# Optimization experiments

Hardware: AMD Instinct MI355X
Metric: run time of the kernel (lower is better)

## Reference

```python
import jax, jax.numpy as jnp
import numpy as np

IN_F, HID, OUT_F, N_HID = 3, 5, 1, 256
OMEGA0 = 30.0


def setup_inputs() -> dict:
    key = jax.random.key(0)
    ks = jax.random.split(key, 7)
    N = 524288
    coords = jax.random.uniform(ks[0], (N, IN_F), dtype=jnp.float32, minval=-1.0, maxval=1.0)
    # first layer init: U(-1/in, 1/in)
    W_first = jax.random.uniform(ks[1], (HID, IN_F), dtype=jnp.float32,
                                 minval=-1.0 / IN_F, maxval=1.0 / IN_F)
    b_first = jax.random.uniform(ks[2], (HID,), dtype=jnp.float32, minval=-1.0, maxval=1.0) / np.sqrt(IN_F)
    # hidden layers: U(-sqrt(6/in)/omega, sqrt(6/in)/omega)
    bnd = np.sqrt(6.0 / HID) / OMEGA0
    W_hidden = jax.random.uniform(ks[3], (N_HID, HID, HID), dtype=jnp.float32, minval=-bnd, maxval=bnd)
    b_hidden = jax.random.uniform(ks[4], (N_HID, HID), dtype=jnp.float32, minval=-1.0, maxval=1.0) / np.sqrt(HID)
    W_final = jax.random.uniform(ks[5], (OUT_F, HID), dtype=jnp.float32, minval=-bnd, maxval=bnd)
    b_final = jax.random.uniform(ks[6], (OUT_F,), dtype=jnp.float32, minval=-1.0, maxval=1.0) / np.sqrt(HID)
    return {"coords": coords, "W_first": W_first, "b_first": b_first,
            "W_hidden": W_hidden, "b_hidden": b_hidden,
            "W_final": W_final, "b_final": b_final}


def siren_forward(coords, W_first, b_first, W_hidden, b_hidden, W_final, b_final):
    # first SineLayer
    x = jnp.sin(OMEGA0 * (coords @ W_first.T + b_first))  # [N, HID]

    # 256 hidden SineLayers via scan over stacked weights
    def step(x, wb):
        w, b = wb  # w: [HID, HID], b: [HID]
        return jnp.sin(OMEGA0 * (x @ w.T + b)), None

    x, _ = jax.lax.scan(step, x, (W_hidden, b_hidden))
    # outermost linear (no sine)
    return x @ W_final.T + b_final  # [N, OUT_F]


def reference(coords, W_first, b_first, W_hidden, b_hidden, W_final, b_final):
    out = siren_forward(coords, W_first, b_first, W_hidden, b_hidden, W_final, b_final)
    # torch module returns (output, coords); coords is just the input passthrough
    return (out, coords)
```

## Files before the change

### kernel.cpp

```cpp
#include <hip/hip_runtime.h>
#include <math.h>


#define SIREN_HID 5
#define SIREN_NLAYERS 256

#define SIREN_REV 4.774648292756860f

__device__ __forceinline__ float siren_sin30(float z) {
    float t = z * SIREN_REV;
    return __builtin_amdgcn_sinf(__builtin_amdgcn_fractf(t));
}

__global__ __launch_bounds__(256)
void siren_fwd(const float* __restrict__ coords,
               const float* __restrict__ Wf,
               const float* __restrict__ bf,
               const float* __restrict__ Wh,
               const float* __restrict__ bh,
               const float* __restrict__ Wfin,
               const float* __restrict__ bfin,
               float* __restrict__ out, int N)
{
    int i = blockIdx.x * blockDim.x + threadIdx.x;
    if (i >= N) return;

    float c0 = coords[3 * i + 0];
    float c1 = coords[3 * i + 1];
    float c2 = coords[3 * i + 2];

    float h0, h1, h2, h3, h4;
    {
        float t0 = fmaf(c2, Wf[0 * 3 + 2], fmaf(c1, Wf[0 * 3 + 1], fmaf(c0, Wf[0 * 3 + 0], bf[0])));
        float t1 = fmaf(c2, Wf[1 * 3 + 2], fmaf(c1, Wf[1 * 3 + 1], fmaf(c0, Wf[1 * 3 + 0], bf[1])));
        float t2 = fmaf(c2, Wf[2 * 3 + 2], fmaf(c1, Wf[2 * 3 + 1], fmaf(c0, Wf[2 * 3 + 0], bf[2])));
        float t3 = fmaf(c2, Wf[3 * 3 + 2], fmaf(c1, Wf[3 * 3 + 1], fmaf(c0, Wf[3 * 3 + 0], bf[3])));
        float t4 = fmaf(c2, Wf[4 * 3 + 2], fmaf(c1, Wf[4 * 3 + 1], fmaf(c0, Wf[4 * 3 + 0], bf[4])));
        h0 = siren_sin30(t0);
        h1 = siren_sin30(t1);
        h2 = siren_sin30(t2);
        h3 = siren_sin30(t3);
        h4 = siren_sin30(t4);
    }

#pragma unroll 4
    for (int l = 0; l < SIREN_NLAYERS; ++l) {
        const float* w = Wh + l * (SIREN_HID * SIREN_HID);
        const float* b = bh + l * SIREN_HID;
        float t0 = fmaf(h4, w[ 4], fmaf(h3, w[ 3], fmaf(h2, w[ 2], fmaf(h1, w[ 1], fmaf(h0, w[ 0], b[0])))));
        float t1 = fmaf(h4, w[ 9], fmaf(h3, w[ 8], fmaf(h2, w[ 7], fmaf(h1, w[ 6], fmaf(h0, w[ 5], b[1])))));
        float t2 = fmaf(h4, w[14], fmaf(h3, w[13], fmaf(h2, w[12], fmaf(h1, w[11], fmaf(h0, w[10], b[2])))));
        float t3 = fmaf(h4, w[19], fmaf(h3, w[18], fmaf(h2, w[17], fmaf(h1, w[16], fmaf(h0, w[15], b[3])))));
        float t4 = fmaf(h4, w[24], fmaf(h3, w[23], fmaf(h2, w[22], fmaf(h1, w[21], fmaf(h0, w[20], b[4])))));
        h0 = siren_sin30(t0);
        h1 = siren_sin30(t1);
        h2 = siren_sin30(t2);
        h3 = siren_sin30(t3);
        h4 = siren_sin30(t4);
    }

    float o = fmaf(h4, Wfin[4], fmaf(h3, Wfin[3], fmaf(h2, Wfin[2], fmaf(h1, Wfin[1], fmaf(h0, Wfin[0], bfin[0])))));
    out[i] = o;

    float* oc = out + N;
    oc[3 * i + 0] = c0;
    oc[3 * i + 1] = c1;
    oc[3 * i + 2] = c2;
}

extern "C" void kernel_launch(void* const* d_in, const int* in_sizes, int n_in,
                              void* d_out, int out_size, void* d_ws, size_t ws_size,
                              hipStream_t stream) {
    const float* coords = (const float*)d_in[0];
    const float* Wf     = (const float*)d_in[1];
    const float* bf     = (const float*)d_in[2];
    const float* Wh     = (const float*)d_in[3];
    const float* bh     = (const float*)d_in[4];
    const float* Wfin   = (const float*)d_in[5];
    const float* bfin   = (const float*)d_in[6];

    int N = in_sizes[0] / 3;
    float* out = (float*)d_out;

    dim3 block(256);
    dim3 grid((N + 255) / 256);
    hipLaunchKernelGGL(siren_fwd, grid, block, 0, stream,
                       coords, Wf, bf, Wh, bh, Wfin, bfin, out, N);
}
```

Measured before the change: 170.8 us.

## Prescale weights by omega/2pi in a prep kernel and process two points per thread

A new prep kernel folds the omega0/(2π) factor into all first-layer and hidden weights and biases. It stores them in a workspace padded to 32 floats per layer. The main kernel then calls the hardware sin directly on the pre-activations, dropping the per-neuron multiply and fract. Each thread now evaluates two coordinates, which shares the weight loads and raises instruction-level parallelism, but it adds a second kernel launch and relies on v_sin handling unreduced arguments within its valid range.

```diff
diff --git a/kernel.cpp b/kernel.cpp
--- a/kernel.cpp
+++ b/kernel.cpp
@@ -4,68 +4,100 @@
 
 #define SIREN_HID 5
 #define SIREN_NLAYERS 256
-
 #define SIREN_REV 4.774648292756860f
 
-__device__ __forceinline__ float siren_sin30(float z) {
-    float t = z * SIREN_REV;
-    return __builtin_amdgcn_sinf(__builtin_amdgcn_fractf(t));
+__global__ __launch_bounds__(256)
+void siren_prep(const float* __restrict__ Wf, const float* __restrict__ bf,
+                const float* __restrict__ Wh, const float* __restrict__ bh,
+                float* __restrict__ ws)
+{
+    int t = blockIdx.x * blockDim.x + threadIdx.x;
+    const int total = SIREN_NLAYERS * 32;
+    for (int idx = t; idx < total; idx += gridDim.x * blockDim.x) {
+        int l = idx >> 5;
+        int k = idx & 31;
+        float v = 0.0f;
+        if (k < 25)      v = Wh[l * 25 + k] * SIREN_REV;
+        else if (k < 30) v = bh[l * 5 + (k - 25)] * SIREN_REV;
+        ws[idx] = v;
+    }
+    if (t < 15) ws[total + t]      = Wf[t] * SIREN_REV;
+    if (t < 5)  ws[total + 15 + t] = bf[t] * SIREN_REV;
 }
 
 __global__ __launch_bounds__(256)
-void siren_fwd(const float* __restrict__ coords,
-               const float* __restrict__ Wf,
-               const float* __restrict__ bf,
-               const float* __restrict__ Wh,
-               const float* __restrict__ bh,
-               const float* __restrict__ Wfin,
-               const float* __restrict__ bfin,
-               float* __restrict__ out, int N)
+void siren_fwd3(const float* __restrict__ coords,
+                const float* __restrict__ lw,
+                const float* __restrict__ fw,
+                const float* __restrict__ Wfin,
+                const float* __restrict__ bfin,
+                float* __restrict__ out, int N)
 {
     int i = blockIdx.x * blockDim.x + threadIdx.x;
-    if (i >= N) return;
+    const int M = N >> 1;
+    i = (i < M) ? i : (M - 1);
 
-    float c0 = coords[3 * i + 0];
-    float c1 = coords[3 * i + 1];
-    float c2 = coords[3 * i + 2];
+    const float* cp = coords + 6 * i;
+    float a0 = cp[0], a1 = cp[1], a2 = cp[2];
+    float b0 = cp[3], b1 = cp[4], b2 = cp[5];
 
-    float h0, h1, h2, h3, h4;
+    float ha0, ha1, ha2, ha3, ha4;
+    float hb0, hb1, hb2, hb3, hb4;
     {
-        float t0 = fmaf(c2, Wf[0 * 3 + 2], fmaf(c1, Wf[0 * 3 + 1], fmaf(c0, Wf[0 * 3 + 0], bf[0])));
-        float t1 = fmaf(c2, Wf[1 * 3 + 2], fmaf(c1, Wf[1 * 3 + 1], fmaf(c0, Wf[1 * 3 + 0], bf[1])));
-        float t2 = fmaf(c2, Wf[2 * 3 + 2], fmaf(c1, Wf[2 * 3 + 1], fmaf(c0, Wf[2 * 3 + 0], bf[2])));
-        float t3 = fmaf(c2, Wf[3 * 3 + 2], fmaf(c1, Wf[3 * 3 + 1], fmaf(c0, Wf[3 * 3 + 0], bf[3])));
-        float t4 = fmaf(c2, Wf[4 * 3 + 2], fmaf(c1, Wf[4 * 3 + 1], fmaf(c0, Wf[4 * 3 + 0], bf[4])));
-        h0 = siren_sin30(t0);
-        h1 = siren_sin30(t1);
-        h2 = siren_sin30(t2);
-        h3 = siren_sin30(t3);
-        h4 = siren_sin30(t4);
+        float s0 = fw[ 0], s1 = fw[ 1], s2 = fw[ 2], t0 = fw[15];
+        float s3 = fw[ 3], s4 = fw[ 4], s5 = fw[ 5], t1 = fw[16];
+        float s6 = fw[ 6], s7 = fw[ 7], s8 = fw[ 8], t2 = fw[17];
+        float s9 = fw[ 9], sA = fw[10], sB = fw[11], t3 = fw[18];
+        float sC = fw[12], sD = fw[13], sE = fw[14], t4 = fw[19];
+        float za0 = fmaf(a2, s2, fmaf(a1, s1, fmaf(a0, s0, t0)));
+        float za1 = fmaf(a2, s5, fmaf(a1, s4, fmaf(a0, s3, t1)));
+        float za2 = fmaf(a2, s8, fmaf(a1, s7, fmaf(a0, s6, t2)));
+        float za3 = fmaf(a2, sB, fmaf(a1, sA, fmaf(a0, s9, t3)));
+        float za4 = fmaf(a2, sE, fmaf(a1, sD, fmaf(a0, sC, t4)));
+        float zb0 = fmaf(b2, s2, fmaf(b1, s1, fmaf(b0, s0, t0)));
+        float zb1 = fmaf(b2, s5, fmaf(b1, s4, fmaf(b0, s3, t1)));
+        float zb2 = fmaf(b2, s8, fmaf(b1, s7, fmaf(b0, s6, t2)));
+        float zb3 = fmaf(b2, sB, fmaf(b1, sA, fmaf(b0, s9, t3)));
+        float zb4 = fmaf(b2, sE, fmaf(b1, sD, fmaf(b0, sC, t4)));
+        ha0 = __builtin_amdgcn_sinf(za0); hb0 = __builtin_amdgcn_sinf(zb0);
+        ha1 = __builtin_amdgcn_sinf(za1); hb1 = __builtin_amdgcn_sinf(zb1);
+        ha2 = __builtin_amdgcn_sinf(za2); hb2 = __builtin_amdgcn_sinf(zb2);
+        ha3 = __builtin_amdgcn_sinf(za3); hb3 = __builtin_amdgcn_sinf(zb3);
+        ha4 = __builtin_amdgcn_sinf(za4); hb4 = __builtin_amdgcn_sinf(zb4);
     }
 
-#pragma unroll 4
+#pragma unroll 2
     for (int l = 0; l < SIREN_NLAYERS; ++l) {
-        const float* w = Wh + l * (SIREN_HID * SIREN_HID);
-        const float* b = bh + l * SIREN_HID;
-        float t0 = fmaf(h4, w[ 4], fmaf(h3, w[ 3], fmaf(h2, w[ 2], fmaf(h1, w[ 1], fmaf(h0, w[ 0], b[0])))));
-        float t1 = fmaf(h4, w[ 9], fmaf(h3, w[ 8], fmaf(h2, w[ 7], fmaf(h1, w[ 6], fmaf(h0, w[ 5], b[1])))));
-        float t2 = fmaf(h4, w[14], fmaf(h3, w[13], fmaf(h2, w[12], fmaf(h1, w[11], fmaf(h0, w[10], b[2])))));
-        float t3 = fmaf(h4, w[19], fmaf(h3, w[18], fmaf(h2, w[17], fmaf(h1, w[16], fmaf(h0, w[15], b[3])))));
-        float t4 = fmaf(h4, w[24], fmaf(h3, w[23], fmaf(h2, w[22], fmaf(h1, w[21], fmaf(h0, w[20], b[4])))));
-        h0 = siren_sin30(t0);
-        h1 = siren_sin30(t1);
-        h2 = siren_sin30(t2);
-        h3 = siren_sin30(t3);
-        h4 = siren_sin30(t4);
+        const float* w = lw + l * 32;
+        float p0 = w[25], p1 = w[26], p2 = w[27], p3 = w[28], p4 = w[29];
+        float za0 = fmaf(ha4, w[ 4], fmaf(ha3, w[ 3], fmaf(ha2, w[ 2], fmaf(ha1, w[ 1], fmaf(ha0, w[ 0], p0)))));
+        float zb0 = fmaf(hb4, w[ 4], fmaf(hb3, w[ 3], fmaf(hb2, w[ 2], fmaf(hb1, w[ 1], fmaf(hb0, w[ 0], p0)))));
+        float za1 = fmaf(ha4, w[ 9], fmaf(ha3, w[ 8], fmaf(ha2, w[ 7], fmaf(ha1, w[ 6], fmaf(ha0, w[ 5], p1)))));
+        float zb1 = fmaf(hb4, w[ 9], fmaf(hb3, w[ 8], fmaf(hb2, w[ 7], fmaf(hb1, w[ 6], fmaf(hb0, w[ 5], p1)))));
+        float za2 = fmaf(ha4, w[14], fmaf(ha3, w[13], fmaf(ha2, w[12], fmaf(ha1, w[11], fmaf(ha0, w[10], p2)))));
+        float zb2 = fmaf(hb4, w[14], fmaf(hb3, w[13], fmaf(hb2, w[12], fmaf(hb1, w[11], fmaf(hb0, w[10], p2)))));
+        float za3 = fmaf(ha4, w[19], fmaf(ha3, w[18], fmaf(ha2, w[17], fmaf(ha1, w[16], fmaf(ha0, w[15], p3)))));
+        float zb3 = fmaf(hb4, w[19], fmaf(hb3, w[18], fmaf(hb2, w[17], fmaf(hb1, w[16], fmaf(hb0, w[15], p3)))));
+        float za4 = fmaf(ha4, w[24], fmaf(ha3, w[23], fmaf(ha2, w[22], fmaf(ha1, w[21], fmaf(ha0, w[20], p4)))));
+        float zb4 = fmaf(hb4, w[24], fmaf(hb3, w[23], fmaf(hb2, w[22], fmaf(hb1, w[21], fmaf(hb0, w[20], p4)))));
+        ha0 = __builtin_amdgcn_sinf(za0); hb0 = __builtin_amdgcn_sinf(zb0);
+        ha1 = __builtin_amdgcn_sinf(za1); hb1 = __builtin_amdgcn_sinf(zb1);
+        ha2 = __builtin_amdgcn_sinf(za2); hb2 = __builtin_amdgcn_sinf(zb2);
+        ha3 = __builtin_amdgcn_sinf(za3); hb3 = __builtin_amdgcn_sinf(zb3);
+        ha4 = __builtin_amdgcn_sinf(za4); hb4 = __builtin_amdgcn_sinf(zb4);
     }
 
-    float o = fmaf(h4, Wfin[4], fmaf(h3, Wfin[3], fmaf(h2, Wfin[2], fmaf(h1, Wfin[1], fmaf(h0, Wfin[0], bfin[0])))));
-    out[i] = o;
+    float w0 = Wfin[0], w1 = Wfin[1], w2 = Wfin[2], w3 = Wfin[3], w4 = Wfin[4];
+    float bb = bfin[0];
+    float oa = fmaf(ha4, w4, fmaf(ha3, w3, fmaf(ha2, w2, fmaf(ha1, w1, fmaf(ha0, w0, bb)))));
+    float ob = fmaf(hb4, w4, fmaf(hb3, w3, fmaf(hb2, w2, fmaf(hb1, w1, fmaf(hb0, w0, bb)))));
 
-    float* oc = out + N;
-    oc[3 * i + 0] = c0;
-    oc[3 * i + 1] = c1;
-    oc[3 * i + 2] = c2;
+    out[2 * i + 0] = oa;
+    out[2 * i + 1] = ob;
+
+    float* oc = out + N + 6 * i;
+    oc[0] = a0; oc[1] = a1; oc[2] = a2;
+    oc[3] = b0; oc[4] = b1; oc[5] = b2;
 }
 
 extern "C" void kernel_launch(void* const* d_in, const int* in_sizes, int n_in,
@@ -81,9 +113,13 @@
 
     int N = in_sizes[0] / 3;
     float* out = (float*)d_out;
+    float* ws = (float*)d_ws;
 
+    hipLaunchKernelGGL(siren_prep, dim3(32), dim3(256), 0, stream, Wf, bf, Wh, bh, ws);
+
+    int M = N / 2;
     dim3 block(256);
-    dim3 grid((N + 255) / 256);
-    hipLaunchKernelGGL(siren_fwd, grid, block, 0, stream,
-                       coords, Wf, bf, Wh, bh, Wfin, bfin, out, N);
+    dim3 grid((M + 255) / 256);
+    hipLaunchKernelGGL(siren_fwd3, grid, block, 0, stream,
+                       coords, ws, ws + SIREN_NLAYERS * 32, Wfin, bfin, out, N);
 }
```

After: 163.1 us. 4.5% less time.
